# Kernel optimization log

Hardware: AMD Instinct MI355X
Metric: run time of the kernel (lower is better)

## Reference

```python
import jax, jax.numpy as jnp
import numpy as np

DIM = 256
HEADS = 8


def _ln(x, g, b, eps=1e-5):
    mu = jnp.mean(x, axis=-1, keepdims=True)
    var = jnp.var(x, axis=-1, keepdims=True)
    return (x - mu) * jax.lax.rsqrt(var + eps) * g + b


def setup_inputs() -> dict:
    key = jax.random.key(0)
    ks = jax.random.split(key, 12)
    d = DIM
    s = lambda fan: 1.0 / np.sqrt(fan)
    return {
        "x": jax.random.normal(ks[0], (1, d, 64, 64), dtype=jnp.float32),
        "ln1_g": jnp.ones((d,), jnp.float32),
        "ln1_b": jnp.zeros((d,), jnp.float32),
        "w_qkv": jax.random.normal(ks[1], (3 * d, d), jnp.float32) * s(d),
        "b_qkv": jnp.zeros((3 * d,), jnp.float32),
        "w_proj": jax.random.normal(ks[2], (d, d), jnp.float32) * s(d),
        "b_proj": jnp.zeros((d,), jnp.float32),
        "ln2_g": jnp.ones((d,), jnp.float32),
        "ln2_b": jnp.zeros((d,), jnp.float32),
        "w_mlp1": jax.random.normal(ks[3], (4 * d, d), jnp.float32) * s(d),
        "b_mlp1": jnp.zeros((4 * d,), jnp.float32),
        "w_mlp2": jax.random.normal(ks[4], (d, 4 * d), jnp.float32) * s(4 * d),
        "b_mlp2": jnp.zeros((d,), jnp.float32),
    }


def reference(x, ln1_g, ln1_b, w_qkv, b_qkv, w_proj, b_proj,
              ln2_g, ln2_b, w_mlp1, b_mlp1, w_mlp2, b_mlp2):
    B, C, H, W = x.shape
    hd = HEADS
    d = C // hd
    scale = d ** (-0.5)
    # work channels-last: [B, H, W, C] -> [B, HW, C]
    xl = jnp.transpose(x, (0, 2, 3, 1)).reshape(B, H * W, C)

    # --- attention branch ---
    xn = _ln(xl, ln1_g, ln1_b)
    qkv = jnp.einsum('bnc,oc->bno', xn, w_qkv) + b_qkv  # [B, N, 3C]
    q, k, v = jnp.split(qkv, 3, axis=-1)
    def heads(t):  # [B,N,C] -> [B,h,N,d]
        return jnp.transpose(t.reshape(B, H * W, hd, d), (0, 2, 1, 3))
    q, k, v = heads(q), heads(k), heads(v)
    attn = jax.nn.softmax(jnp.einsum('bhnd,bhmd->bhnm', q, k) * scale, axis=-1)
    out = jnp.einsum('bhnm,bhmd->bhnd', attn, v)  # [B,h,N,d]
    out = jnp.transpose(out, (0, 2, 1, 3)).reshape(B, H * W, C)
    xl = xl + jnp.einsum('bnc,oc->bno', out, w_proj) + b_proj

    # --- MLP branch ---
    xn = _ln(xl, ln2_g, ln2_b)
    h1 = jax.nn.gelu(jnp.einsum('bnc,oc->bno', xn, w_mlp1) + b_mlp1,
                     approximate=False)
    xl = xl + jnp.einsum('bnf,of->bno', h1, w_mlp2) + b_mlp2

    return jnp.transpose(xl.reshape(B, H, W, C), (0, 3, 1, 2))
```

## Files before the change

kernel.cpp:

```cpp
#include <hip/hip_runtime.h>
#include <hip/hip_bf16.h>

typedef __bf16 bf16_t;
typedef __bf16 bf16x8 __attribute__((ext_vector_type(8)));
typedef __bf16 bf16x4 __attribute__((ext_vector_type(4)));
typedef float  f32x4  __attribute__((ext_vector_type(4)));
typedef unsigned int uint;

#define MFMA(a,b,c) __builtin_amdgcn_mfma_f32_16x16x32_bf16((a),(b),(c),0,0,0)

__device__ __forceinline__ size_t pidx(int n, int k, int K) {
  return (size_t)(n >> 4) * (K << 4) + ((k >> 3) << 7) + ((n & 15) << 3) + (k & 7);
}

__device__ __forceinline__ uint packbf2(float lo, float hi) {
  unsigned short a = __builtin_bit_cast(unsigned short, (bf16_t)lo);
  unsigned short b = __builtin_bit_cast(unsigned short, (bf16_t)hi);
  return (uint)a | ((uint)b << 16);
}

__global__ __launch_bounds__(256) void cvt_pack_all(const float* __restrict__ w_qkv,
                                                    const float* __restrict__ w_proj,
                                                    const float* __restrict__ w_mlp1,
                                                    const float* __restrict__ w_mlp2,
                                                    bf16_t* __restrict__ wq, bf16_t* __restrict__ wp,
                                                    bf16_t* __restrict__ w1, bf16_t* __restrict__ w2) {
  int b = blockIdx.x;
  const float* src; bf16_t* dst; int t0, ksh;
  if (b < 96)       { src = w_qkv;  dst = wq; ksh = 5; t0 = b * 256; }
  else if (b < 128) { src = w_proj; dst = wp; ksh = 5; t0 = (b - 96) * 256; }
  else if (b < 256) { src = w_mlp1; dst = w1; ksh = 5; t0 = (b - 128) * 256; }
  else              { src = w_mlp2; dst = w2; ksh = 7; t0 = (b - 256) * 256; }
  int t = t0 + threadIdx.x;
  int n = t >> ksh, kb = t & ((1 << ksh) - 1);
  int K = 8 << ksh;
  const float* p = src + (size_t)n * K + kb * 8;
  float4 a = *(const float4*)p;
  float4 c = *(const float4*)(p + 4);
  bf16x8 o = {(bf16_t)a.x, (bf16_t)a.y, (bf16_t)a.z, (bf16_t)a.w,
              (bf16_t)c.x, (bf16_t)c.y, (bf16_t)c.z, (bf16_t)c.w};
  *(bf16x8*)(dst + (size_t)(n >> 4) * (K << 4) + kb * 128 + ((n & 15) << 3)) = o;
}

__global__ __launch_bounds__(256) void fused_in(const float* __restrict__ x,
                                                const float* __restrict__ g,
                                                const float* __restrict__ bta,
                                                float* __restrict__ xl,
                                                bf16_t* __restrict__ xn) {
  __shared__ float tile[256][33];
  __shared__ float psum[8][32], psq[8][32], mu_s[32], rs_s[32];
  int t = threadIdx.x, n0 = blockIdx.x * 32;
  int lane32 = t & 31, grp = t >> 5;
#pragma unroll
  for (int it = 0; it < 32; ++it) {
    int c = grp + it * 8;
    tile[c][lane32] = x[(size_t)c * 4096 + n0 + lane32];
  }
  __syncthreads();
  float s = 0.f, sq = 0.f;
#pragma unroll
  for (int ci = 0; ci < 32; ++ci) {
    float v = tile[grp * 32 + ci][lane32];
    s += v; sq += v * v;
  }
  psum[grp][lane32] = s; psq[grp][lane32] = sq;
  __syncthreads();
  if (t < 32) {
    float S = 0.f, Q = 0.f;
#pragma unroll
    for (int p = 0; p < 8; ++p) { S += psum[p][t]; Q += psq[p][t]; }
    float mu = S * (1.0f / 256.0f);
    float var = Q * (1.0f / 256.0f) - mu * mu;
    mu_s[t] = mu; rs_s[t] = rsqrtf(var + 1e-5f);
  }
  __syncthreads();
  {
    float mu = mu_s[lane32], rs = rs_s[lane32];
    int row = n0 + lane32;
    bf16_t* op = xn + (size_t)(row >> 4) * 4096 + ((row & 15) << 3);
#pragma unroll
    for (int cc8 = 0; cc8 < 4; ++cc8) {
      int c0 = grp * 32 + cc8 * 8;
      bf16x8 o;
#pragma unroll
      for (int j = 0; j < 8; ++j) {
        int c = c0 + j;
        o[j] = (bf16_t)((tile[c][lane32] - mu) * rs * g[c] + bta[c]);
      }
      *(bf16x8*)(op + ((c0 >> 3) << 7)) = o;
    }
  }
#pragma unroll
  for (int it = 0; it < 4; ++it) {
    int j = grp + it * 8;
#pragma unroll
    for (int c0 = 0; c0 < 256; c0 += 32)
      xl[(size_t)(n0 + j) * 256 + c0 + lane32] = tile[c0 + lane32][j];
  }
}

template <int K, int EPI, int RPW, int KS = 1>
__global__ __launch_bounds__(256) void gemm_bt(const bf16_t* __restrict__ A,
                                               const bf16_t* __restrict__ W,
                                               const float* __restrict__ bias,
                                               void* __restrict__ outp, int ldn) {
  constexpr int RB = RPW / 16;
  constexpr int KLEN = K / KS;
  int w = threadIdx.x >> 6, lane = threadIdx.x & 63;
  int quad = lane >> 4, idx = lane & 15;
  int row0 = blockIdx.x * (4 * RPW) + w * RPW;
  int col0 = blockIdx.y * 64;
  int kb0 = (KS > 1) ? blockIdx.z * KLEN : 0;
  f32x4 acc[RB][4];
#pragma unroll
  for (int rb = 0; rb < RB; ++rb)
#pragma unroll
    for (int nb = 0; nb < 4; ++nb) acc[rb][nb] = (f32x4){0.f, 0.f, 0.f, 0.f};
  const bf16_t* abase = A + (size_t)(row0 >> 4) * (K << 4) + quad * 128 + idx * 8;
  const bf16_t* wbase = W + (size_t)(col0 >> 4) * (K << 4) + quad * 128 + idx * 8;
#pragma unroll 4
  for (int k0 = kb0; k0 < kb0 + KLEN; k0 += 32) {
    bf16x8 a[RB];
#pragma unroll
    for (int rb = 0; rb < RB; ++rb)
      a[rb] = *(const bf16x8*)(abase + (size_t)rb * (K << 4) + k0 * 16);
#pragma unroll
    for (int nb = 0; nb < 4; ++nb) {
      bf16x8 b = *(const bf16x8*)(wbase + (size_t)nb * (K << 4) + k0 * 16);
#pragma unroll
      for (int rb = 0; rb < RB; ++rb) acc[rb][nb] = MFMA(a[rb], b, acc[rb][nb]);
    }
  }
#pragma unroll
  for (int nb = 0; nb < 4; ++nb) {
    int c = col0 + nb * 16 + idx;
    float bv = (EPI == 4) ? 0.f : bias[c];
#pragma unroll
    for (int rb = 0; rb < RB; ++rb)
#pragma unroll
      for (int r = 0; r < 4; ++r) {
        int rr = row0 + rb * 16 + quad * 4 + r;
        float v = acc[rb][nb][r] + bv;
        if constexpr (EPI == 1) {
          float z = v * (0.7978845608f + 0.0356774081f * v * v);
          float t = __builtin_amdgcn_exp2f(z * 2.885390082f);
          float th = 1.f - 2.f * __builtin_amdgcn_rcpf(t + 1.f);
          v = 0.5f * v * (1.f + th);
          ((bf16_t*)outp)[pidx(rr, c, ldn)] = (bf16_t)v;
        } else if constexpr (EPI == 4) {
          ((float*)outp)[((size_t)blockIdx.z * 4096 + rr) * ldn + c] = v;
        } else {
          bf16_t* qh = (bf16_t*)outp;
          bf16_t* kh = qh + 1048576;
          bf16_t* vp = kh + 1048576;
          if (c < 256) {
            qh[(size_t)(c >> 5) * 131072 + rr * 32 + (c & 31)] = (bf16_t)v;
          } else if (c < 512) {
            kh[(size_t)((c - 256) >> 5) * 131072 + rr * 32 + (c & 31)] = (bf16_t)v;
          } else {
            vp[(size_t)((c - 512) >> 5) * 131072 + (rr >> 5) * 1024 + (c & 31) * 32 + (rr & 31)] = (bf16_t)v;
          }
        }
      }
  }
}

#define SPLIT 4
__global__ __launch_bounds__(256, 4) void attn_split(const bf16_t* __restrict__ qkvh,
                                                     uint* __restrict__ o_part,
                                                     float* __restrict__ l_part) {
  __shared__ bf16_t P[2][4][32][72];
  int w = threadIdx.x >> 6, lane = threadIdx.x & 63;
  int quad = lane >> 4, idx = lane & 15;
  int qt = blockIdx.x & 31;
  int h  = (blockIdx.x >> 5) & 7;
  int sp = blockIdx.x >> 8;
  int qrow = qt * 128 + w * 32;
  const bf16_t* qh = qkvh + (size_t)h * 131072;
  const bf16_t* kh = qh + 8 * 131072;
  const bf16_t* vp = kh + 8 * 131072;
  const float cs = 0.25503518f;
  bf16x8 qr0 = *(const bf16x8*)(qh + (size_t)(qrow + idx) * 32 + quad * 8);
  bf16x8 qr1 = *(const bf16x8*)(qh + (size_t)(qrow + 16 + idx) * 32 + quad * 8);
  bf16x8 qf0, qf1;
#pragma unroll
  for (int j = 0; j < 8; ++j) {
    qf0[j] = (bf16_t)((float)qr0[j] * cs);
    qf1[j] = (bf16_t)((float)qr1[j] * cs);
  }
  float ls0 = 0.f, ls1 = 0.f;
  f32x4 o00 = {0.f,0.f,0.f,0.f}, o01 = {0.f,0.f,0.f,0.f};
  f32x4 o10 = {0.f,0.f,0.f,0.f}, o11 = {0.f,0.f,0.f,0.f};
  const f32x4 zero = {0.f,0.f,0.f,0.f};
  int kbase = sp * 1024;

  bf16x8 kf[4];
#pragma unroll
  for (int kb = 0; kb < 4; ++kb)
    kf[kb] = *(const bf16x8*)(kh + (size_t)(kbase + kb * 16 + idx) * 32 + quad * 8);

#pragma unroll
  for (int kb = 0; kb < 4; ++kb) {
    f32x4 s0 = MFMA(kf[kb], qf0, zero);
    f32x4 s1 = MFMA(kf[kb], qf1, zero);
    float a0 = __builtin_amdgcn_exp2f(s0[0]), a1 = __builtin_amdgcn_exp2f(s0[1]);
    float a2 = __builtin_amdgcn_exp2f(s0[2]), a3 = __builtin_amdgcn_exp2f(s0[3]);
    float b0 = __builtin_amdgcn_exp2f(s1[0]), b1 = __builtin_amdgcn_exp2f(s1[1]);
    float b2 = __builtin_amdgcn_exp2f(s1[2]), b3 = __builtin_amdgcn_exp2f(s1[3]);
    ls0 += (a0 + a1) + (a2 + a3);
    ls1 += (b0 + b1) + (b2 + b3);
    bf16x4 pk0 = {(bf16_t)a0, (bf16_t)a1, (bf16_t)a2, (bf16_t)a3};
    bf16x4 pk1 = {(bf16_t)b0, (bf16_t)b1, (bf16_t)b2, (bf16_t)b3};
    *(bf16x4*)&P[0][w][idx][kb * 16 + quad * 4] = pk0;
    *(bf16x4*)&P[0][w][16 + idx][kb * 16 + quad * 4] = pk1;
  }
#pragma unroll
  for (int kb = 0; kb < 4; ++kb)
    kf[kb] = *(const bf16x8*)(kh + (size_t)(kbase + 64 + kb * 16 + idx) * 32 + quad * 8);

#pragma unroll 2
  for (int t = 0; t < 16; ++t) {
    int par = t & 1;
    int k0 = kbase + t * 64;
    bf16x8 pa00 = *(const bf16x8*)&P[par][w][idx][quad * 8];
    bf16x8 pa01 = *(const bf16x8*)&P[par][w][idx][32 + quad * 8];
    bf16x8 pa10 = *(const bf16x8*)&P[par][w][16 + idx][quad * 8];
    bf16x8 pa11 = *(const bf16x8*)&P[par][w][16 + idx][32 + quad * 8];
    const bf16_t* vt = vp + (size_t)(k0 >> 5) * 1024 + quad * 8;
    bf16x8 vv0 = *(const bf16x8*)(vt + idx * 32);
    bf16x8 vv1 = *(const bf16x8*)(vt + (idx + 16) * 32);
    bf16x8 vv2 = *(const bf16x8*)(vt + 1024 + idx * 32);
    bf16x8 vv3 = *(const bf16x8*)(vt + 1024 + (idx + 16) * 32);
    int kn = kbase + ((t + 2) & 15) * 64;
    bf16x8 kfn[4];
#pragma unroll
    for (int kb = 0; kb < 4; ++kb)
      kfn[kb] = *(const bf16x8*)(kh + (size_t)(kn + kb * 16 + idx) * 32 + quad * 8);
    if (t < 15) {
#pragma unroll
      for (int kb = 0; kb < 4; ++kb) {
        f32x4 s0 = MFMA(kf[kb], qf0, zero);
        f32x4 s1 = MFMA(kf[kb], qf1, zero);
        float a0 = __builtin_amdgcn_exp2f(s0[0]), a1 = __builtin_amdgcn_exp2f(s0[1]);
        float a2 = __builtin_amdgcn_exp2f(s0[2]), a3 = __builtin_amdgcn_exp2f(s0[3]);
        float b0 = __builtin_amdgcn_exp2f(s1[0]), b1 = __builtin_amdgcn_exp2f(s1[1]);
        float b2 = __builtin_amdgcn_exp2f(s1[2]), b3 = __builtin_amdgcn_exp2f(s1[3]);
        ls0 += (a0 + a1) + (a2 + a3);
        ls1 += (b0 + b1) + (b2 + b3);
        bf16x4 pk0 = {(bf16_t)a0, (bf16_t)a1, (bf16_t)a2, (bf16_t)a3};
        bf16x4 pk1 = {(bf16_t)b0, (bf16_t)b1, (bf16_t)b2, (bf16_t)b3};
        *(bf16x4*)&P[1 - par][w][idx][kb * 16 + quad * 4] = pk0;
        *(bf16x4*)&P[1 - par][w][16 + idx][kb * 16 + quad * 4] = pk1;
      }
    }
    o00 = MFMA(pa00, vv0, o00);
    o01 = MFMA(pa00, vv1, o01);
    o10 = MFMA(pa10, vv0, o10);
    o11 = MFMA(pa10, vv1, o11);
    o00 = MFMA(pa01, vv2, o00);
    o01 = MFMA(pa01, vv3, o01);
    o10 = MFMA(pa11, vv2, o10);
    o11 = MFMA(pa11, vv3, o11);
#pragma unroll
    for (int kb = 0; kb < 4; ++kb) kf[kb] = kfn[kb];
  }
  ls0 += __shfl_xor(ls0, 16); ls0 += __shfl_xor(ls0, 32);
  ls1 += __shfl_xor(ls1, 16); ls1 += __shfl_xor(ls1, 32);
  if (quad == 0) {
    l_part[((size_t)sp * 8 + h) * 4096 + qrow + idx]      = ls0;
    l_part[((size_t)sp * 8 + h) * 4096 + qrow + 16 + idx] = ls1;
  }
#pragma unroll
  for (int r = 0; r < 4; ++r) {
    int n0 = qrow + quad * 4 + r;
    o_part[(((size_t)sp * 4096 + n0) * 8 + h) * 16 + idx] = packbf2(o00[r], o01[r]);
    int n1 = n0 + 16;
    o_part[(((size_t)sp * 4096 + n1) * 8 + h) * 16 + idx] = packbf2(o10[r], o11[r]);
  }
}

__global__ __launch_bounds__(256) void attn_norm(const uint* __restrict__ o_part,
                                                 const float* __restrict__ l_part,
                                                 bf16_t* __restrict__ attn) {
  int t = blockIdx.x * 256 + threadIdx.x;
  int j0 = (t & 3) * 4;
  int h  = (t >> 2) & 7;
  int n  = t >> 5;
  float l = 0.f;
#pragma unroll
  for (int s = 0; s < SPLIT; ++s) l += l_part[((size_t)s * 8 + h) * 4096 + n];
  float inv = 1.0f / l;
  float alo[4] = {0.f,0.f,0.f,0.f}, ahi[4] = {0.f,0.f,0.f,0.f};
#pragma unroll
  for (int s = 0; s < SPLIT; ++s) {
    const uint* p = o_part + (((size_t)s * 4096 + n) * 8 + h) * 16 + j0;
    uint4 v = *(const uint4*)p;
    uint vv[4] = {v.x, v.y, v.z, v.w};
#pragma unroll
    for (int jj = 0; jj < 4; ++jj) {
      alo[jj] += __builtin_bit_cast(float, vv[jj] << 16);
      ahi[jj] += __builtin_bit_cast(float, vv[jj] & 0xffff0000u);
    }
  }
  bf16x4 lo = {(bf16_t)(alo[0] * inv), (bf16_t)(alo[1] * inv),
               (bf16_t)(alo[2] * inv), (bf16_t)(alo[3] * inv)};
  bf16x4 hi = {(bf16_t)(ahi[0] * inv), (bf16_t)(ahi[1] * inv),
               (bf16_t)(ahi[2] * inv), (bf16_t)(ahi[3] * inv)};
  int k1 = h * 32 + j0;
  int k2 = k1 + 16;
  *(bf16x4*)(attn + (size_t)(n >> 4) * 4096 + ((k1 >> 3) << 7) + ((n & 15) << 3) + (k1 & 7)) = lo;
  *(bf16x4*)(attn + (size_t)(n >> 4) * 4096 + ((k2 >> 3) << 7) + ((n & 15) << 3) + (k2 & 7)) = hi;
}

__global__ __launch_bounds__(256) void combine_ln(const float* __restrict__ pp,
                                                  const float* __restrict__ xl,
                                                  const float* __restrict__ bias,
                                                  const float* __restrict__ g,
                                                  const float* __restrict__ bta,
                                                  float* __restrict__ xl2,
                                                  bf16_t* __restrict__ xn2) {
  int row  = blockIdx.x * 4 + (threadIdx.x >> 6);
  int lane = threadIdx.x & 63;
  size_t ri = (size_t)row * 64 + lane;
  float4 rr = ((const float4*)xl)[ri];
  float4 bb = ((const float4*)bias)[lane];
  float4 v = {rr.x + bb.x, rr.y + bb.y, rr.z + bb.z, rr.w + bb.w};
#pragma unroll
  for (int s = 0; s < 2; ++s) {
    float4 p = ((const float4*)pp)[ri + (size_t)s * 4096 * 64];
    v.x += p.x; v.y += p.y; v.z += p.z; v.w += p.w;
  }
  ((float4*)xl2)[ri] = v;
  float s  = v.x + v.y + v.z + v.w;
  float sq = v.x * v.x + v.y * v.y + v.z * v.z + v.w * v.w;
#pragma unroll
  for (int off = 32; off; off >>= 1) {
    s  += __shfl_xor(s, off);
    sq += __shfl_xor(sq, off);
  }
  float mu  = s * (1.0f / 256.0f);
  float var = sq * (1.0f / 256.0f) - mu * mu;
  float rs  = rsqrtf(var + 1e-5f);
  float4 gg = ((const float4*)g)[lane];
  float4 b2 = ((const float4*)bta)[lane];
  bf16x4 o = {(bf16_t)((v.x - mu) * rs * gg.x + b2.x),
              (bf16_t)((v.y - mu) * rs * gg.y + b2.y),
              (bf16_t)((v.z - mu) * rs * gg.z + b2.z),
              (bf16_t)((v.w - mu) * rs * gg.w + b2.w)};
  int k = lane * 4;
  *(bf16x4*)(xn2 + (size_t)(row >> 4) * 4096 + ((k >> 3) << 7) + ((row & 15) << 3) + (k & 7)) = o;
}

__global__ __launch_bounds__(256) void combine_transpose(const float* __restrict__ mp,
                                                         const float* __restrict__ xl2,
                                                         const float* __restrict__ bias,
                                                         float* __restrict__ dst) {
  __shared__ float tile[32][33];
  int n0 = blockIdx.x * 32, c0 = blockIdx.y * 32;
  int a = threadIdx.x & 31, b = threadIdx.x >> 5;
  float bv = bias[c0 + a];
#pragma unroll
  for (int i = 0; i < 4; ++i) {
    int n = b + i * 8;
    size_t base = (size_t)(n0 + n) * 256 + c0 + a;
    float v = xl2[base] + bv;
#pragma unroll
    for (int s = 0; s < 4; ++s) v += mp[(size_t)s * 1048576 + base];
    tile[a][n] = v;
  }
  __syncthreads();
#pragma unroll
  for (int i = 0; i < 4; ++i) {
    int c = b + i * 8;
    dst[(size_t)(c0 + c) * 4096 + n0 + a] = tile[c][a];
  }
}

extern "C" void kernel_launch(void* const* d_in, const int* in_sizes, int n_in,
                              void* d_out, int out_size, void* d_ws, size_t ws_size,
                              hipStream_t stream) {
  const float* x      = (const float*)d_in[0];
  const float* ln1_g  = (const float*)d_in[1];
  const float* ln1_b  = (const float*)d_in[2];
  const float* w_qkv  = (const float*)d_in[3];
  const float* b_qkv  = (const float*)d_in[4];
  const float* w_proj = (const float*)d_in[5];
  const float* b_proj = (const float*)d_in[6];
  const float* ln2_g  = (const float*)d_in[7];
  const float* ln2_b  = (const float*)d_in[8];
  const float* w_mlp1 = (const float*)d_in[9];
  const float* b_mlp1 = (const float*)d_in[10];
  const float* w_mlp2 = (const float*)d_in[11];
  const float* b_mlp2 = (const float*)d_in[12];

  char* ws = (char*)d_ws;
  bf16_t* qkvh   = (bf16_t*)(ws + 0);
  float*  xl     = (float*)(ws + (6u << 20));
  bf16_t* xn     = (bf16_t*)(ws + (10u << 20));
  uint*   o_part = (uint*)(ws + (12u << 20));
  bf16_t* attn   = (bf16_t*)(ws + (20u << 20));
  float*  pp     = (float*)(ws + (24u << 20));
  float*  xl2    = (float*)(ws + (10u << 20));
  bf16_t* xn2    = (bf16_t*)(ws + (14u << 20));
  bf16_t* h1     = (bf16_t*)(ws + 0);
  float*  mp     = (float*)(ws + (16u << 20));
  bf16_t* wq     = (bf16_t*)(ws + (32u << 20));
  bf16_t* wp     = wq + 196608;
  bf16_t* w1     = wp + 65536;
  bf16_t* w2     = w1 + 262144;
  float*  l_part = (float*)(ws + (34304u << 10));

  cvt_pack_all<<<384, 256, 0, stream>>>(w_qkv, w_proj, w_mlp1, w_mlp2, wq, wp, w1, w2);
  fused_in<<<128, 256, 0, stream>>>(x, ln1_g, ln1_b, xl, xn);

  gemm_bt<256, 3, 16><<<dim3(64, 12), 256, 0, stream>>>(xn, wq, b_qkv, qkvh, 768);
  attn_split<<<256 * SPLIT, 256, 0, stream>>>(qkvh, o_part, l_part);
  attn_norm<<<512, 256, 0, stream>>>(o_part, l_part, attn);

  gemm_bt<256, 4, 16, 2><<<dim3(64, 4, 2), 256, 0, stream>>>(attn, wp, nullptr, pp, 256);
  combine_ln<<<1024, 256, 0, stream>>>(pp, xl, b_proj, ln2_g, ln2_b, xl2, xn2);

  gemm_bt<256, 1, 16><<<dim3(64, 16), 256, 0, stream>>>(xn2, w1, b_mlp1, h1, 1024);
  gemm_bt<1024, 4, 16, 4><<<dim3(64, 4, 4), 256, 0, stream>>>(h1, w2, nullptr, mp, 256);
  combine_transpose<<<dim3(128, 8), 256, 0, stream>>>(mp, xl2, b_mlp2, (float*)d_out);
}
```

Baseline: 176.8 us.

## Merge weight pack with input LN kernel and simplify attention P pipeline

Folds the weight conversion/packing kernel and the input transpose+LayerNorm kernel into a single launch, removing one kernel launch. In the attention kernel, drops the double-buffered P staging (software-pipelined QK^T one tile ahead) in favour of a single buffer computed and consumed in the same iteration, which halves shared memory per block. It also reorders block indexing so heads vary fastest, changing which blocks run together and how K/V are reused through cache. The simpler loop loses overlap between exp and PV MFMAs but may raise occupancy.

```diff
diff --git a/kernel.cpp b/kernel.cpp
--- a/kernel.cpp
+++ b/kernel.cpp
@@ -19,37 +19,38 @@
   return (uint)a | ((uint)b << 16);
 }
 
-__global__ __launch_bounds__(256) void cvt_pack_all(const float* __restrict__ w_qkv,
-                                                    const float* __restrict__ w_proj,
-                                                    const float* __restrict__ w_mlp1,
-                                                    const float* __restrict__ w_mlp2,
-                                                    bf16_t* __restrict__ wq, bf16_t* __restrict__ wp,
-                                                    bf16_t* __restrict__ w1, bf16_t* __restrict__ w2) {
-  int b = blockIdx.x;
-  const float* src; bf16_t* dst; int t0, ksh;
-  if (b < 96)       { src = w_qkv;  dst = wq; ksh = 5; t0 = b * 256; }
-  else if (b < 128) { src = w_proj; dst = wp; ksh = 5; t0 = (b - 96) * 256; }
-  else if (b < 256) { src = w_mlp1; dst = w1; ksh = 5; t0 = (b - 128) * 256; }
-  else              { src = w_mlp2; dst = w2; ksh = 7; t0 = (b - 256) * 256; }
-  int t = t0 + threadIdx.x;
-  int n = t >> ksh, kb = t & ((1 << ksh) - 1);
-  int K = 8 << ksh;
-  const float* p = src + (size_t)n * K + kb * 8;
-  float4 a = *(const float4*)p;
-  float4 c = *(const float4*)(p + 4);
-  bf16x8 o = {(bf16_t)a.x, (bf16_t)a.y, (bf16_t)a.z, (bf16_t)a.w,
-              (bf16_t)c.x, (bf16_t)c.y, (bf16_t)c.z, (bf16_t)c.w};
-  *(bf16x8*)(dst + (size_t)(n >> 4) * (K << 4) + kb * 128 + ((n & 15) << 3)) = o;
-}
-
-__global__ __launch_bounds__(256) void fused_in(const float* __restrict__ x,
-                                                const float* __restrict__ g,
-                                                const float* __restrict__ bta,
-                                                float* __restrict__ xl,
-                                                bf16_t* __restrict__ xn) {
+__global__ __launch_bounds__(256) void prep(const float* __restrict__ w_qkv,
+                                            const float* __restrict__ w_proj,
+                                            const float* __restrict__ w_mlp1,
+                                            const float* __restrict__ w_mlp2,
+                                            bf16_t* __restrict__ wq, bf16_t* __restrict__ wp,
+                                            bf16_t* __restrict__ w1, bf16_t* __restrict__ w2,
+                                            const float* __restrict__ x,
+                                            const float* __restrict__ g,
+                                            const float* __restrict__ bta,
+                                            float* __restrict__ xl,
+                                            bf16_t* __restrict__ xn) {
   __shared__ float tile[256][33];
   __shared__ float psum[8][32], psq[8][32], mu_s[32], rs_s[32];
-  int t = threadIdx.x, n0 = blockIdx.x * 32;
+  int b = blockIdx.x;
+  if (b < 384) {
+    const float* src; bf16_t* dst; int t0, ksh;
+    if (b < 96)       { src = w_qkv;  dst = wq; ksh = 5; t0 = b * 256; }
+    else if (b < 128) { src = w_proj; dst = wp; ksh = 5; t0 = (b - 96) * 256; }
+    else if (b < 256) { src = w_mlp1; dst = w1; ksh = 5; t0 = (b - 128) * 256; }
+    else              { src = w_mlp2; dst = w2; ksh = 7; t0 = (b - 256) * 256; }
+    int t = t0 + threadIdx.x;
+    int n = t >> ksh, kb = t & ((1 << ksh) - 1);
+    int K = 8 << ksh;
+    const float* p = src + (size_t)n * K + kb * 8;
+    float4 a = *(const float4*)p;
+    float4 c = *(const float4*)(p + 4);
+    bf16x8 o = {(bf16_t)a.x, (bf16_t)a.y, (bf16_t)a.z, (bf16_t)a.w,
+                (bf16_t)c.x, (bf16_t)c.y, (bf16_t)c.z, (bf16_t)c.w};
+    *(bf16x8*)(dst + (size_t)(n >> 4) * (K << 4) + kb * 128 + ((n & 15) << 3)) = o;
+    return;
+  }
+  int t = threadIdx.x, n0 = (b - 384) * 32;
   int lane32 = t & 31, grp = t >> 5;
 #pragma unroll
   for (int it = 0; it < 32; ++it) {
@@ -169,11 +170,11 @@
 __global__ __launch_bounds__(256, 4) void attn_split(const bf16_t* __restrict__ qkvh,
                                                      uint* __restrict__ o_part,
                                                      float* __restrict__ l_part) {
-  __shared__ bf16_t P[2][4][32][72];
+  __shared__ bf16_t P[4][32][72];
   int w = threadIdx.x >> 6, lane = threadIdx.x & 63;
   int quad = lane >> 4, idx = lane & 15;
-  int qt = blockIdx.x & 31;
-  int h  = (blockIdx.x >> 5) & 7;
+  int h  = blockIdx.x & 7;
+  int qt = (blockIdx.x >> 3) & 31;
   int sp = blockIdx.x >> 8;
   int qrow = qt * 128 + w * 32;
   const bf16_t* qh = qkvh + (size_t)h * 131072;
@@ -199,68 +200,44 @@
   for (int kb = 0; kb < 4; ++kb)
     kf[kb] = *(const bf16x8*)(kh + (size_t)(kbase + kb * 16 + idx) * 32 + quad * 8);
 
-#pragma unroll
-  for (int kb = 0; kb < 4; ++kb) {
-    f32x4 s0 = MFMA(kf[kb], qf0, zero);
-    f32x4 s1 = MFMA(kf[kb], qf1, zero);
-    float a0 = __builtin_amdgcn_exp2f(s0[0]), a1 = __builtin_amdgcn_exp2f(s0[1]);
-    float a2 = __builtin_amdgcn_exp2f(s0[2]), a3 = __builtin_amdgcn_exp2f(s0[3]);
-    float b0 = __builtin_amdgcn_exp2f(s1[0]), b1 = __builtin_amdgcn_exp2f(s1[1]);
-    float b2 = __builtin_amdgcn_exp2f(s1[2]), b3 = __builtin_amdgcn_exp2f(s1[3]);
-    ls0 += (a0 + a1) + (a2 + a3);
-    ls1 += (b0 + b1) + (b2 + b3);
-    bf16x4 pk0 = {(bf16_t)a0, (bf16_t)a1, (bf16_t)a2, (bf16_t)a3};
-    bf16x4 pk1 = {(bf16_t)b0, (bf16_t)b1, (bf16_t)b2, (bf16_t)b3};
-    *(bf16x4*)&P[0][w][idx][kb * 16 + quad * 4] = pk0;
-    *(bf16x4*)&P[0][w][16 + idx][kb * 16 + quad * 4] = pk1;
-  }
-#pragma unroll
-  for (int kb = 0; kb < 4; ++kb)
-    kf[kb] = *(const bf16x8*)(kh + (size_t)(kbase + 64 + kb * 16 + idx) * 32 + quad * 8);
-
-#pragma unroll 2
-  for (int t = 0; t < 16; ++t) {
-    int par = t & 1;
-    int k0 = kbase + t * 64;
-    bf16x8 pa00 = *(const bf16x8*)&P[par][w][idx][quad * 8];
-    bf16x8 pa01 = *(const bf16x8*)&P[par][w][idx][32 + quad * 8];
-    bf16x8 pa10 = *(const bf16x8*)&P[par][w][16 + idx][quad * 8];
-    bf16x8 pa11 = *(const bf16x8*)&P[par][w][16 + idx][32 + quad * 8];
+  for (int kt = 0; kt < 16; ++kt) {
+    int k0 = kbase + kt * 64;
+    int k1 = kbase + ((kt + 1) & 15) * 64;
     const bf16_t* vt = vp + (size_t)(k0 >> 5) * 1024 + quad * 8;
     bf16x8 vv0 = *(const bf16x8*)(vt + idx * 32);
     bf16x8 vv1 = *(const bf16x8*)(vt + (idx + 16) * 32);
     bf16x8 vv2 = *(const bf16x8*)(vt + 1024 + idx * 32);
     bf16x8 vv3 = *(const bf16x8*)(vt + 1024 + (idx + 16) * 32);
-    int kn = kbase + ((t + 2) & 15) * 64;
     bf16x8 kfn[4];
 #pragma unroll
     for (int kb = 0; kb < 4; ++kb)
-      kfn[kb] = *(const bf16x8*)(kh + (size_t)(kn + kb * 16 + idx) * 32 + quad * 8);
-    if (t < 15) {
-#pragma unroll
-      for (int kb = 0; kb < 4; ++kb) {
-        f32x4 s0 = MFMA(kf[kb], qf0, zero);
-        f32x4 s1 = MFMA(kf[kb], qf1, zero);
-        float a0 = __builtin_amdgcn_exp2f(s0[0]), a1 = __builtin_amdgcn_exp2f(s0[1]);
-        float a2 = __builtin_amdgcn_exp2f(s0[2]), a3 = __builtin_amdgcn_exp2f(s0[3]);
-        float b0 = __builtin_amdgcn_exp2f(s1[0]), b1 = __builtin_amdgcn_exp2f(s1[1]);
-        float b2 = __builtin_amdgcn_exp2f(s1[2]), b3 = __builtin_amdgcn_exp2f(s1[3]);
-        ls0 += (a0 + a1) + (a2 + a3);
-        ls1 += (b0 + b1) + (b2 + b3);
-        bf16x4 pk0 = {(bf16_t)a0, (bf16_t)a1, (bf16_t)a2, (bf16_t)a3};
-        bf16x4 pk1 = {(bf16_t)b0, (bf16_t)b1, (bf16_t)b2, (bf16_t)b3};
-        *(bf16x4*)&P[1 - par][w][idx][kb * 16 + quad * 4] = pk0;
-        *(bf16x4*)&P[1 - par][w][16 + idx][kb * 16 + quad * 4] = pk1;
-      }
+      kfn[kb] = *(const bf16x8*)(kh + (size_t)(k1 + kb * 16 + idx) * 32 + quad * 8);
+#pragma unroll
+    for (int kb = 0; kb < 4; ++kb) {
+      f32x4 s0 = MFMA(kf[kb], qf0, zero);
+      f32x4 s1 = MFMA(kf[kb], qf1, zero);
+      float a0 = __builtin_amdgcn_exp2f(s0[0]), a1 = __builtin_amdgcn_exp2f(s0[1]);
+      float a2 = __builtin_amdgcn_exp2f(s0[2]), a3 = __builtin_amdgcn_exp2f(s0[3]);
+      float b0 = __builtin_amdgcn_exp2f(s1[0]), b1 = __builtin_amdgcn_exp2f(s1[1]);
+      float b2 = __builtin_amdgcn_exp2f(s1[2]), b3 = __builtin_amdgcn_exp2f(s1[3]);
+      ls0 += (a0 + a1) + (a2 + a3);
+      ls1 += (b0 + b1) + (b2 + b3);
+      bf16x4 pk0 = {(bf16_t)a0, (bf16_t)a1, (bf16_t)a2, (bf16_t)a3};
+      bf16x4 pk1 = {(bf16_t)b0, (bf16_t)b1, (bf16_t)b2, (bf16_t)b3};
+      *(bf16x4*)&P[w][idx][kb * 16 + quad * 4] = pk0;
+      *(bf16x4*)&P[w][16 + idx][kb * 16 + quad * 4] = pk1;
     }
-    o00 = MFMA(pa00, vv0, o00);
-    o01 = MFMA(pa00, vv1, o01);
-    o10 = MFMA(pa10, vv0, o10);
-    o11 = MFMA(pa10, vv1, o11);
-    o00 = MFMA(pa01, vv2, o00);
-    o01 = MFMA(pa01, vv3, o01);
-    o10 = MFMA(pa11, vv2, o10);
-    o11 = MFMA(pa11, vv3, o11);
+#pragma unroll
+    for (int kc = 0; kc < 2; ++kc) {
+      bf16x8 pa0 = *(const bf16x8*)&P[w][idx][kc * 32 + quad * 8];
+      bf16x8 pa1 = *(const bf16x8*)&P[w][16 + idx][kc * 32 + quad * 8];
+      bf16x8 va = kc ? vv2 : vv0;
+      bf16x8 vb = kc ? vv3 : vv1;
+      o00 = MFMA(pa0, va, o00);
+      o01 = MFMA(pa0, vb, o01);
+      o10 = MFMA(pa1, va, o10);
+      o11 = MFMA(pa1, vb, o11);
+    }
 #pragma unroll
     for (int kb = 0; kb < 4; ++kb) kf[kb] = kfn[kb];
   }
@@ -410,8 +387,8 @@
   bf16_t* w2     = w1 + 262144;
   float*  l_part = (float*)(ws + (34304u << 10));
 
-  cvt_pack_all<<<384, 256, 0, stream>>>(w_qkv, w_proj, w_mlp1, w_mlp2, wq, wp, w1, w2);
-  fused_in<<<128, 256, 0, stream>>>(x, ln1_g, ln1_b, xl, xn);
+  prep<<<512, 256, 0, stream>>>(w_qkv, w_proj, w_mlp1, w_mlp2, wq, wp, w1, w2,
+                                x, ln1_g, ln1_b, xl, xn);
 
   gemm_bt<256, 3, 16><<<dim3(64, 12), 256, 0, stream>>>(xn, wq, b_qkv, qkvh, 768);
   attn_split<<<256 * SPLIT, 256, 0, stream>>>(qkvh, o_part, l_part);
```

Measured after the change: 166.9 us, median of 2. 1.06x faster.
